# Optimization experiments

Measured on AMD Instinct MI355X. Metric: run time of the kernel, lower is better.

## Reference

```python
import jax, jax.numpy as jnp
import numpy as np

B, S0 = 16, 511
D = 512    # encoder_output_dim
HG = 256   # graph_rnn_hidden_graph
HE = 256   # graph_rnn_hidden_edge (must equal HG: h_prev[0] = graph_state)
T = 128    # tag_representation_dim
M = 32     # graph_rnn_m
S = S0 + 1 # after head-sentinel prepend


def setup_inputs() -> dict:
    ks = iter(jax.random.split(jax.random.key(0), 40))
    def U(shape, fan):
        # torch RNN/Linear default init: U(-1/sqrt(fan), 1/sqrt(fan))
        return jax.random.uniform(next(ks), shape, jnp.float32, -1.0, 1.0) / np.sqrt(fan)
    return {
        'input': jax.random.normal(next(ks), (B, S0, D), jnp.float32),
        'sentinel': jax.random.normal(next(ks), (D,), jnp.float32),
        'g_Wih0': U((HG, D), HG), 'g_Whh0': U((HG, HG), HG), 'g_bih0': U((HG,), HG), 'g_bhh0': U((HG,), HG),
        'g_Wih1': U((HG, HG), HG), 'g_Whh1': U((HG, HG), HG), 'g_bih1': U((HG,), HG), 'g_bhh1': U((HG,), HG),
        'e_Wih0': U((HE, 1), HE), 'e_Whh0': U((HE, HE), HE), 'e_bih0': U((HE,), HE), 'e_bhh0': U((HE,), HE),
        'e_Wih1': U((HE, HE), HE), 'e_Whh1': U((HE, HE), HE), 'e_bih1': U((HE,), HE), 'e_bhh1': U((HE,), HE),
        'cls_W': U((1, HE), HE), 'cls_b': U((1,), HE),
        'head_W': U((T, HG), HG), 'head_b': U((T,), HG),
        'dep_W': U((T, HG), HG), 'dep_b': U((T,), HG),
        'mask': jnp.ones((B, S0), jnp.int32),
        'head_indices': jax.random.randint(next(ks), (B, S0), 0, S0, jnp.int32),
    }


def _rnn_layer(x, W_ih, W_hh, b_ih, b_hh):
    # Elman RNN layer (tanh), batch_first, h0 = 0. x: [B, S, Din] -> [B, S, H]
    xw = jnp.einsum('bsd,hd->bsh', x, W_ih) + b_ih + b_hh  # hoist input GEMM out of scan
    h0 = jnp.zeros((x.shape[0], W_hh.shape[0]), x.dtype)
    def step(h, xw_t):
        h = jnp.tanh(xw_t + h @ W_hh.T)
        return h, h
    _, ys = jax.lax.scan(step, h0, jnp.swapaxes(xw, 0, 1))
    return jnp.swapaxes(ys, 0, 1)


def _forward(input, sentinel, g_Wih0, g_Whh0, g_bih0, g_bhh0, g_Wih1, g_Whh1, g_bih1, g_bhh1,
             e_Wih0, e_Whh0, e_bih0, e_bhh0, e_Wih1, e_Whh1, e_bih1, e_bhh1,
             cls_W, cls_b, head_W, head_b, dep_W, dep_b, mask, head_indices):
    Bv = input.shape[0]
    # prepend head sentinel / prepend_ones
    x = jnp.concatenate([jnp.broadcast_to(sentinel, (Bv, 1, D)), input], axis=1)   # [B,S,D]
    mask_f = jnp.concatenate([jnp.ones((Bv, 1), mask.dtype), mask], axis=1)        # [B,S]
    # graph_pass: 2-layer tanh RNN; pad_packed_sequence zeroes padded timesteps
    h = _rnn_layer(x, g_Wih0, g_Whh0, g_bih0, g_bhh0)
    gs = _rnn_layer(h, g_Wih1, g_Whh1, g_bih1, g_bhh1)                             # [B,S,HG]
    gs = gs * mask_f[..., None].astype(gs.dtype)
    N = Bv * S
    gt = gs.reshape(N, HG)
    def estep(carry, _):
        xe, h0, h1 = carry
        h0 = jnp.tanh(xe @ e_Wih0.T + e_bih0 + e_bhh0 + h0 @ e_Whh0.T)
        h1 = jnp.tanh(h0 @ e_Wih1.T + e_bih1 + e_bhh1 + h1 @ e_Whh1.T)
        p = jax.nn.sigmoid(h1 @ cls_W.T + cls_b)   # [N,1]
        return (p, h0, h1), p[:, 0]
    init = (jnp.ones((N, 1), gs.dtype), gt, jnp.zeros((N, HE), gs.dtype))
    _, probs = jax.lax.scan(estep, init, None, length=M)                           # [M,N]
    A = jnp.concatenate([jnp.ones((1, N), gs.dtype), probs], axis=0).T.reshape(Bv, S, M + 1)
    # reshape_adj: scatter the M-band back into a [B,S,S] matrix, then transpose
    Ab = A[:, :, 1:]                                                               # [B,S,M]
    i = jnp.arange(S)[:, None]
    j = jnp.arange(S)[None, :]
    start = jnp.maximum(0, i - M)
    valid = (j >= start) & (j < i)
    midx = jnp.clip(j - start, 0, M - 1)                                           # [S,S]
    gathered = Ab[:, jnp.arange(S)[:, None], midx]                                 # [B,S,S]
    arc_logits = jnp.swapaxes(jnp.where(valid[None], gathered, jnp.zeros((), gs.dtype)), 1, 2)
    # tag heads (dropout = identity at inference)
    head_tag = jax.nn.elu(jnp.einsum('bsh,th->bst', gs, head_W) + head_b)
    dep_tag = jax.nn.elu(jnp.einsum('bsh,th->bst', gs, dep_W) + dep_b)
    return head_tag, dep_tag, arc_logits


def reference(input, sentinel, g_Wih0, g_Whh0, g_bih0, g_bhh0, g_Wih1, g_Whh1, g_bih1, g_bhh1,
              e_Wih0, e_Whh0, e_bih0, e_bhh0, e_Wih1, e_Whh1, e_bih1, e_bhh1,
              cls_W, cls_b, head_W, head_b, dep_W, dep_b, mask, head_indices):
    return _forward(input, sentinel, g_Wih0, g_Whh0, g_bih0, g_bhh0, g_Wih1, g_Whh1, g_bih1, g_bhh1,
                    e_Wih0, e_Whh0, e_bih0, e_bhh0, e_Wih1, e_Whh1, e_bih1, e_bhh1,
                    cls_W, cls_b, head_W, head_b, dep_W, dep_b, mask, head_indices)
```

## Files before the change

### kernel.cpp

```cpp
#include <hip/hip_runtime.h>

typedef unsigned short u16;
typedef short s8v __attribute__((ext_vector_type(8)));
typedef float f4v __attribute__((ext_vector_type(4)));

__device__ __forceinline__ float bf2f(u16 s) {
  unsigned u = ((unsigned)s) << 16;
  return __builtin_bit_cast(float, u);
}
__device__ __forceinline__ u16 f2bf(float f) {
  unsigned u = __builtin_bit_cast(unsigned, f);
  unsigned r = u + 0x7fffu + ((u >> 16) & 1u);
  return (u16)(r >> 16);
}
__device__ __forceinline__ s8v load8bf(const u16* p) {
  return __builtin_bit_cast(s8v, *(const uint4*)p);
}
__device__ __forceinline__ f4v mfma16(s8v a, s8v b, f4v c) {
  return __builtin_amdgcn_mfma_f32_16x16x32_bf16(a, b, c, 0, 0, 0);
}
__device__ __forceinline__ s8v pin8(s8v x) {
  union { s8v v; unsigned u[4]; } t;
  t.v = x;
  asm volatile("" : "+v"(t.u[0]), "+v"(t.u[1]), "+v"(t.u[2]), "+v"(t.u[3]));
  return t.v;
}
__device__ __forceinline__ void barrier_lds() {
  asm volatile("s_waitcnt lgkmcnt(0)\n\ts_barrier" ::: "memory");
}
__device__ __forceinline__ void cvt8(const float* p, s8v& hi, s8v& lo) {
  float4 x0 = ((const float4*)p)[0];
  float4 x1 = ((const float4*)p)[1];
  float v[8] = {x0.x, x0.y, x0.z, x0.w, x1.x, x1.y, x1.z, x1.w};
  union { s8v v; u16 a[8]; } H, L;
#pragma unroll
  for (int i = 0; i < 8; ++i) {
    u16 h = f2bf(v[i]);
    H.a[i] = h;
    L.a[i] = f2bf(v[i] - bf2f(h));
  }
  hi = H.v;
  lo = L.v;
}
__device__ __forceinline__ float fast_tanh(float x) {
  float t = __builtin_amdgcn_exp2f(x * 2.885390081777927f);
  return 1.f - 2.f * __builtin_amdgcn_rcpf(t + 1.f);
}
__device__ __forceinline__ float fast_sigmoid(float x) {
  float t = __builtin_amdgcn_exp2f(x * -1.4426950408889634f);
  return __builtin_amdgcn_rcpf(1.f + t);
}

__global__ void k_prep(const float* __restrict__ W0, const float* __restrict__ W1,
                       u16* __restrict__ whh0b, u16* __restrict__ whh1b,
                       const float* __restrict__ E0, const float* __restrict__ E1,
                       const float* __restrict__ E2, u16* __restrict__ B0,
                       u16* __restrict__ B1, u16* __restrict__ B2,
                       const float* __restrict__ gW0, u16* __restrict__ gw0hi,
                       u16* __restrict__ gw0lo, const float* __restrict__ gW1,
                       u16* __restrict__ gw1hi, u16* __restrict__ gw1lo,
                       const float* __restrict__ hW, u16* __restrict__ hWhi,
                       u16* __restrict__ hWlo, const float* __restrict__ dW,
                       u16* __restrict__ dWhi, u16* __restrict__ dWlo,
                       const int* __restrict__ mask, float* __restrict__ maskfb) {
  int t = blockIdx.x * 256 + threadIdx.x;
  if (t < 131072) {
    int layer = t >> 16;
    int idx = t & 65535;
    const float* W = layer ? W1 : W0;
    u16* dst = layer ? whh1b : whh0b;
    dst[idx] = f2bf(W[idx]);
  } else if (t < 327680) {
    int c = t - 131072;
    int which = c >> 16;
    int idx = c & 65535;
    const float* src = which == 0 ? E0 : (which == 1 ? E1 : E2);
    u16* dst = which == 0 ? B0 : (which == 1 ? B1 : B2);
    dst[idx] = f2bf(src[idx]);
  } else if (t < 589824) {
    const float* src;
    u16 *dhi, *dlo;
    int idx;
    if (t < 458752) { idx = t - 327680; src = gW0; dhi = gw0hi; dlo = gw0lo; }
    else if (t < 524288) { idx = t - 458752; src = gW1; dhi = gw1hi; dlo = gw1lo; }
    else if (t < 557056) { idx = t - 524288; src = hW; dhi = hWhi; dlo = hWlo; }
    else { idx = t - 557056; src = dW; dhi = dWhi; dlo = dWlo; }
    float v = src[idx];
    u16 h = f2bf(v);
    dhi[idx] = h;
    dlo[idx] = f2bf(v - bf2f(h));
  } else if (t < 598016) {
    int c = t - 589824;
    int s = c >> 4, b = c & 15;
    maskfb[c] = (s == 0) ? 1.f : (float)mask[b * 511 + s - 1];
  }
}

__launch_bounds__(256)
__global__ void k_xw0(const float* __restrict__ input, const float* __restrict__ sentinel,
                      const u16* __restrict__ Whi, const u16* __restrict__ Wlo,
                      const float* __restrict__ b1, const float* __restrict__ b2,
                      float* __restrict__ outxw) {
  const int l = threadIdx.x & 63;
  const int wv = threadIdx.x >> 6;
  const int l15 = l & 15, q = l >> 4;
  const int row0 = blockIdx.x * 64 + wv * 16;
  const int col0 = blockIdx.y * 64;
  int row = row0 + l15;
  int s = row & 511, b = row >> 9;
  const float* aptr = (s == 0) ? sentinel : input + (((size_t)(b * 511 + s - 1)) << 9);
  f4v acc[4];
#pragma unroll
  for (int i = 0; i < 4; ++i) acc[i] = (f4v){0.f, 0.f, 0.f, 0.f};
#pragma unroll
  for (int kt = 0; kt < 16; ++kt) {
    int k0 = kt * 32 + q * 8;
    s8v ah, al;
    cvt8(aptr + k0, ah, al);
#pragma unroll
    for (int nt = 0; nt < 4; ++nt) {
      int j = col0 + nt * 16 + l15;
      s8v wh = load8bf(Whi + ((size_t)j << 9) + k0);
      s8v wl = load8bf(Wlo + ((size_t)j << 9) + k0);
      acc[nt] = mfma16(ah, wh, acc[nt]);
      acc[nt] = mfma16(al, wh, acc[nt]);
      acc[nt] = mfma16(ah, wl, acc[nt]);
    }
  }
#pragma unroll
  for (int nt = 0; nt < 4; ++nt) {
    int col = col0 + nt * 16 + l15;
    float bias = b1[col] + b2[col];
#pragma unroll
    for (int r = 0; r < 4; ++r) {
      int rr = row0 + q * 4 + r;
      outxw[((size_t)rr << 8) + col] = acc[nt][r] + bias;
    }
  }
}

__launch_bounds__(256)
__global__ void k_gemm(const float* __restrict__ A, const u16* __restrict__ Whi,
                       const u16* __restrict__ Wlo, const float* __restrict__ b1,
                       const float* __restrict__ b2, float* __restrict__ outf,
                       int K, int J, int act) {
  const int l = threadIdx.x & 63;
  const int wv = threadIdx.x >> 6;
  const int l15 = l & 15, q = l >> 4;
  const int row0 = blockIdx.x * 64 + wv * 16;
  const int col0 = blockIdx.y * 64;
  const float* aptr = A + (size_t)(row0 + l15) * K;
  f4v acc[4];
#pragma unroll
  for (int i = 0; i < 4; ++i) acc[i] = (f4v){0.f, 0.f, 0.f, 0.f};
  const int nkt = K >> 5;
  for (int kt = 0; kt < nkt; ++kt) {
    int k0 = kt * 32 + q * 8;
    s8v ah, al;
    cvt8(aptr + k0, ah, al);
#pragma unroll
    for (int nt = 0; nt < 4; ++nt) {
      int j = col0 + nt * 16 + l15;
      s8v wh = load8bf(Whi + (size_t)j * K + k0);
      s8v wl = load8bf(Wlo + (size_t)j * K + k0);
      acc[nt] = mfma16(ah, wh, acc[nt]);
      acc[nt] = mfma16(al, wh, acc[nt]);
      acc[nt] = mfma16(ah, wl, acc[nt]);
    }
  }
#pragma unroll
  for (int nt = 0; nt < 4; ++nt) {
    int col = col0 + nt * 16 + l15;
    float bias = b1[col] + (b2 ? b2[col] : 0.f);
#pragma unroll
    for (int r = 0; r < 4; ++r) {
      int rr = row0 + q * 4 + r;
      float v = acc[nt][r] + bias;
      if (act) v = v > 0.f ? v : (__builtin_amdgcn_exp2f(v * 1.4426950408889634f) - 1.f);
      outf[(size_t)rr * J + col] = v;
    }
  }
}

__launch_bounds__(256, 1)
__global__ void k_scan_m(const float* __restrict__ xw, const u16* __restrict__ Wb,
                         float* __restrict__ outf, const float* __restrict__ maskf) {
  __shared__ u16 H[2][272];
  __shared__ float mtab[512];
  const int tid = threadIdx.x;
  const int l = tid & 63, wv = tid >> 6;
  const int l15 = l & 15, q = l >> 4;
  const int b = blockIdx.x;

  s8v w[4][8];
#pragma unroll
  for (int nt = 0; nt < 4; ++nt) {
    int j = wv * 64 + nt * 16 + l15;
#pragma unroll
    for (int kt = 0; kt < 8; ++kt)
      w[nt][kt] = pin8(load8bf(Wb + (j << 8) + kt * 32 + q * 8));
  }
  if (tid < 256) H[0][tid] = 0;
  for (int c = tid; c < 512; c += 256)
    mtab[c] = maskf ? maskf[c * 16 + b] : 1.f;
  __syncthreads();

  const size_t nbase = (size_t)b << 9;
  const float* xrow = xw + (nbase << 8);
  const int j0 = wv * 64 + l15;
  const int q0 = (q == 0);

  float xA[4], xB[4];
#pragma unroll
  for (int nt = 0; nt < 4; ++nt) {
    xA[nt] = xrow[j0 + nt * 16];
    xB[nt] = xrow[256 + j0 + nt * 16];
  }

  auto STEP = [&](int s, int par, float* xc) {
    const u16* Hr = &H[par][0];
    f4v acc[4];
#pragma unroll
    for (int nt = 0; nt < 4; ++nt) acc[nt] = (f4v){xc[nt], 0.f, 0.f, 0.f};
#pragma unroll
    for (int kt = 0; kt < 8; ++kt) {
      s8v ha = load8bf(Hr + kt * 32 + q * 8);
#pragma unroll
      for (int nt = 0; nt < 4; ++nt) acc[nt] = mfma16(ha, w[nt][kt], acc[nt]);
    }
    float mf = mtab[s];
    u16* Hw = &H[1 - par][0];
    float* orow = outf + ((nbase + s) << 8);
#pragma unroll
    for (int nt = 0; nt < 4; ++nt) {
      float h = fast_tanh(acc[nt][0]);
      if (q0) {
        Hw[j0 + nt * 16] = f2bf(h);
        orow[j0 + nt * 16] = h * mf;
      }
    }
  };

  for (int s = 0; s < 512; s += 2) {
    STEP(s, 0, xA);
    int sp = s + 2; if (sp > 511) sp = 511;
#pragma unroll
    for (int nt = 0; nt < 4; ++nt) xA[nt] = xrow[(sp << 8) + j0 + nt * 16];
    barrier_lds();
    STEP(s + 1, 1, xB);
    int sq = s + 3; if (sq > 511) sq = 511;
#pragma unroll
    for (int nt = 0; nt < 4; ++nt) xB[nt] = xrow[(sq << 8) + j0 + nt * 16];
    barrier_lds();
  }
}

__launch_bounds__(512, 2)
__global__ void k_enc(const float* __restrict__ gs,
                      const u16* __restrict__ W0b, const u16* __restrict__ W1b,
                      const u16* __restrict__ W2b, const float* __restrict__ wih0,
                      const float* __restrict__ bih0, const float* __restrict__ bhh0,
                      const float* __restrict__ bih1, const float* __restrict__ bhh1,
                      const float* __restrict__ clsW, const float* __restrict__ clsb,
                      float* __restrict__ Ab) {
  __shared__ __align__(16) u16 hA0[32 * 264];
  __shared__ __align__(16) u16 hA1[32 * 264];
  __shared__ float xe[32];
  __shared__ float b0v[256], w0v[256], b1v[256], clsv[256];
  __shared__ float clsbs;
  const int tid = threadIdx.x;
  const int n0 = blockIdx.x * 32;

  for (int c = tid; c < 8192; c += 512) {
    int row = c >> 8, col = c & 255;
    hA0[row * 264 + col] = f2bf(gs[(((size_t)(n0 + row)) << 8) + col]);
    hA1[row * 264 + col] = 0;
  }
  if (tid < 256) {
    b0v[tid] = bih0[tid] + bhh0[tid];
    w0v[tid] = wih0[tid];
    b1v[tid] = bih1[tid] + bhh1[tid];
    clsv[tid] = clsW[tid];
  }
  if (tid < 32) xe[tid] = 1.0f;
  if (tid == 0) clsbs = clsb[0];

  const int l = tid & 63, wv = tid >> 6;
  const int l15 = l & 15, q = l >> 4;
  const int colbase = wv * 32;

  s8v w0[2][8], w1[2][8], w2[2][8];
#pragma unroll
  for (int nt = 0; nt < 2; ++nt) {
    int jj = colbase + nt * 16 + l15;
#pragma unroll
    for (int kt = 0; kt < 8; ++kt) {
      int off = (jj << 8) + kt * 32 + q * 8;
      w0[nt][kt] = load8bf(W0b + off);
      w1[nt][kt] = load8bf(W1b + off);
      w2[nt][kt] = load8bf(W2b + off);
    }
  }
  __syncthreads();

  for (int m = 0; m < 32; ++m) {
    f4v acc[2][2];
#pragma unroll
    for (int mt = 0; mt < 2; ++mt)
#pragma unroll
      for (int nt = 0; nt < 2; ++nt) acc[mt][nt] = (f4v){0.f, 0.f, 0.f, 0.f};
#pragma unroll
    for (int kt = 0; kt < 8; ++kt) {
#pragma unroll
      for (int mt = 0; mt < 2; ++mt) {
        s8v a = __builtin_bit_cast(s8v, *(const uint4*)&hA0[(mt * 16 + l15) * 264 + kt * 32 + q * 8]);
        acc[mt][0] = mfma16(a, w0[0][kt], acc[mt][0]);
        acc[mt][1] = mfma16(a, w0[1][kt], acc[mt][1]);
      }
    }
    __syncthreads();
#pragma unroll
    for (int nt = 0; nt < 2; ++nt) {
      int col = colbase + nt * 16 + l15;
      float wc = w0v[col], bc = b0v[col];
#pragma unroll
      for (int mt = 0; mt < 2; ++mt)
#pragma unroll
        for (int r = 0; r < 4; ++r) {
          int row = mt * 16 + q * 4 + r;
          float v = acc[mt][nt][r] + xe[row] * wc + bc;
          hA0[row * 264 + col] = f2bf(fast_tanh(v));
        }
    }
    __syncthreads();
#pragma unroll
    for (int mt = 0; mt < 2; ++mt)
#pragma unroll
      for (int nt = 0; nt < 2; ++nt) acc[mt][nt] = (f4v){0.f, 0.f, 0.f, 0.f};
#pragma unroll
    for (int kt = 0; kt < 8; ++kt) {
#pragma unroll
      for (int mt = 0; mt < 2; ++mt) {
        s8v a0 = __builtin_bit_cast(s8v, *(const uint4*)&hA0[(mt * 16 + l15) * 264 + kt * 32 + q * 8]);
        s8v a1 = __builtin_bit_cast(s8v, *(const uint4*)&hA1[(mt * 16 + l15) * 264 + kt * 32 + q * 8]);
        acc[mt][0] = mfma16(a0, w1[0][kt], acc[mt][0]);
        acc[mt][1] = mfma16(a0, w1[1][kt], acc[mt][1]);
        acc[mt][0] = mfma16(a1, w2[0][kt], acc[mt][0]);
        acc[mt][1] = mfma16(a1, w2[1][kt], acc[mt][1]);
      }
    }
    __syncthreads();
#pragma unroll
    for (int nt = 0; nt < 2; ++nt) {
      int col = colbase + nt * 16 + l15;
      float bc = b1v[col];
#pragma unroll
      for (int mt = 0; mt < 2; ++mt)
#pragma unroll
        for (int r = 0; r < 4; ++r) {
          int row = mt * 16 + q * 4 + r;
          float v = acc[mt][nt][r] + bc;
          hA1[row * 264 + col] = f2bf(fast_tanh(v));
        }
    }
    __syncthreads();
    if (tid < 256) {
      int row = tid >> 3, seg = tid & 7;
      float sum = 0.f;
#pragma unroll
      for (int u = 0; u < 4; ++u) {
        int col = seg * 32 + u * 8;
#pragma unroll
        for (int e = 0; e < 8; ++e) sum += bf2f(hA1[row * 264 + col + e]) * clsv[col + e];
      }
      sum += __shfl_down(sum, 4, 8);
      sum += __shfl_down(sum, 2, 8);
      sum += __shfl_down(sum, 1, 8);
      if (seg == 0) {
        float pp = fast_sigmoid(sum + clsbs);
        xe[row] = pp;
        Ab[(((size_t)(n0 + row)) << 5) + m] = pp;
      }
    }
    __syncthreads();
  }
}

__global__ void k_arc(const float* __restrict__ Ab, float* __restrict__ out2) {
  int t = blockIdx.x * 256 + threadIdx.x;
  int b = t >> 18;
  int rem = t & 262143;
  int j = rem >> 9, i = rem & 511;
  int start = i - 32;
  if (start < 0) start = 0;
  float v = 0.f;
  if (j >= start && j < i) v = Ab[((((size_t)b << 9) + i) << 5) + (j - start)];
  out2[t] = v;
}

extern "C" void kernel_launch(void* const* d_in, const int* in_sizes, int n_in,
                              void* d_out, int out_size, void* d_ws, size_t ws_size,
                              hipStream_t stream) {
  const float* input    = (const float*)d_in[0];
  const float* sentinel = (const float*)d_in[1];
  const float* g_Wih0   = (const float*)d_in[2];
  const float* g_Whh0   = (const float*)d_in[3];
  const float* g_bih0   = (const float*)d_in[4];
  const float* g_bhh0   = (const float*)d_in[5];
  const float* g_Wih1   = (const float*)d_in[6];
  const float* g_Whh1   = (const float*)d_in[7];
  const float* g_bih1   = (const float*)d_in[8];
  const float* g_bhh1   = (const float*)d_in[9];
  const float* e_Wih0   = (const float*)d_in[10];
  const float* e_Whh0   = (const float*)d_in[11];
  const float* e_bih0   = (const float*)d_in[12];
  const float* e_bhh0   = (const float*)d_in[13];
  const float* e_Wih1   = (const float*)d_in[14];
  const float* e_Whh1   = (const float*)d_in[15];
  const float* e_bih1   = (const float*)d_in[16];
  const float* e_bhh1   = (const float*)d_in[17];
  const float* cls_W    = (const float*)d_in[18];
  const float* cls_b    = (const float*)d_in[19];
  const float* head_W   = (const float*)d_in[20];
  const float* head_b   = (const float*)d_in[21];
  const float* dep_W    = (const float*)d_in[22];
  const float* dep_b    = (const float*)d_in[23];
  const int* mask       = (const int*)d_in[24];

  float* out = (float*)d_out;
  char* ws = (char*)d_ws;
  float* xw_buf = (float*)ws;
  float* hseq   = (float*)(ws + (8u << 20));
  float* gsb    = (float*)(ws + (16u << 20));
  float* Ab     = (float*)(ws + (24u << 20));
  size_t o = (25u << 20);
  u16* whh0b   = (u16*)(ws + o); o += 128u << 10;
  u16* whh1b   = (u16*)(ws + o); o += 128u << 10;
  float* maskfb= (float*)(ws + o); o += 32u << 10;
  u16* eb0     = (u16*)(ws + o); o += 128u << 10;
  u16* eb1     = (u16*)(ws + o); o += 128u << 10;
  u16* eb2     = (u16*)(ws + o); o += 128u << 10;
  u16* gw0hi   = (u16*)(ws + o); o += 256u << 10;
  u16* gw0lo   = (u16*)(ws + o); o += 256u << 10;
  u16* gw1hi   = (u16*)(ws + o); o += 128u << 10;
  u16* gw1lo   = (u16*)(ws + o); o += 128u << 10;
  u16* hWhi    = (u16*)(ws + o); o += 64u << 10;
  u16* hWlo    = (u16*)(ws + o); o += 64u << 10;
  u16* dWhi    = (u16*)(ws + o); o += 64u << 10;
  u16* dWlo    = (u16*)(ws + o); o += 64u << 10;

  k_prep<<<2336, 256, 0, stream>>>(g_Whh0, g_Whh1, whh0b, whh1b, e_Whh0, e_Wih1, e_Whh1,
                                   eb0, eb1, eb2, g_Wih0, gw0hi, gw0lo, g_Wih1, gw1hi,
                                   gw1lo, head_W, hWhi, hWlo, dep_W, dWhi, dWlo,
                                   mask, maskfb);
  k_xw0<<<dim3(128, 4), 256, 0, stream>>>(input, sentinel, gw0hi, gw0lo, g_bih0, g_bhh0,
                                          xw_buf);
  k_scan_m<<<16, 256, 0, stream>>>(xw_buf, whh0b, hseq, nullptr);
  k_gemm<<<dim3(128, 4), 256, 0, stream>>>(hseq, gw1hi, gw1lo, g_bih1, g_bhh1, xw_buf,
                                           256, 256, 0);
  k_scan_m<<<16, 256, 0, stream>>>(xw_buf, whh1b, gsb, maskfb);
  k_gemm<<<dim3(128, 2), 256, 0, stream>>>(gsb, hWhi, hWlo, head_b, nullptr, out,
                                           256, 128, 1);
  k_gemm<<<dim3(128, 2), 256, 0, stream>>>(gsb, dWhi, dWlo, dep_b, nullptr, out + 1048576,
                                           256, 128, 1);
  k_enc<<<256, 512, 0, stream>>>(gsb, eb0, eb1, eb2, e_Wih0, e_bih0, e_bhh0,
                                 e_bih1, e_bhh1, cls_W, cls_b, Ab);
  k_arc<<<16384, 256, 0, stream>>>(Ab, out + 2097152);
}
```

Measured before the change: 961.8 us.

## Fuse both graph RNN layers into one wavefront-pipelined scan kernel

Replaces the two sequential layer scans and the intermediate input-projection GEMM with a single kernel that runs layer 0 and layer 1 in a skewed pipeline. Each step computes layer-0's recurrence, layer-1's input projection from the fresh layer-0 state, and layer-1's recurrence for an earlier timestep, passing values through LDS. This removes one serial 512-step scan and the GEMM plus its global round trip, at the cost of three times the MFMA work per step and triple the register-resident weights, which may raise register pressure. The layer-1 input projection now uses only the high bf16 part of the weights instead of the hi/lo split, lowering precision.

```diff
diff --git a/kernel.cpp b/kernel.cpp
--- a/kernel.cpp
+++ b/kernel.cpp
@@ -183,31 +183,46 @@
 }
 
 __launch_bounds__(256, 1)
-__global__ void k_scan_m(const float* __restrict__ xw, const u16* __restrict__ Wb,
+__global__ void k_scan_f(const float* __restrict__ xw, const u16* __restrict__ W0b,
+                         const u16* __restrict__ Wxb, const u16* __restrict__ W1b,
+                         const float* __restrict__ bih1, const float* __restrict__ bhh1,
                          float* __restrict__ outf, const float* __restrict__ maskf) {
-  __shared__ u16 H[2][272];
+  __shared__ u16 H1[2][272];
+  __shared__ u16 H2[2][272];
+  __shared__ float XW2[2][272];
   __shared__ float mtab[512];
   const int tid = threadIdx.x;
   const int l = tid & 63, wv = tid >> 6;
   const int l15 = l & 15, q = l >> 4;
   const int b = blockIdx.x;
 
-  s8v w[4][8];
+  s8v w0[4][8], wx[4][8], w1[4][8];
 #pragma unroll
   for (int nt = 0; nt < 4; ++nt) {
     int j = wv * 64 + nt * 16 + l15;
 #pragma unroll
-    for (int kt = 0; kt < 8; ++kt)
-      w[nt][kt] = pin8(load8bf(Wb + (j << 8) + kt * 32 + q * 8));
-  }
-  if (tid < 256) H[0][tid] = 0;
-  for (int c = tid; c < 512; c += 256)
-    mtab[c] = maskf ? maskf[c * 16 + b] : 1.f;
+    for (int kt = 0; kt < 8; ++kt) {
+      int off = (j << 8) + kt * 32 + q * 8;
+      w0[nt][kt] = pin8(load8bf(W0b + off));
+      wx[nt][kt] = pin8(load8bf(Wxb + off));
+      w1[nt][kt] = pin8(load8bf(W1b + off));
+    }
+  }
+  if (tid < 256) {
+    H1[0][tid] = 0; H1[1][tid] = 0;
+    H2[0][tid] = 0; H2[1][tid] = 0;
+    XW2[0][tid] = 0.f; XW2[1][tid] = 0.f;
+  }
+  for (int c = tid; c < 512; c += 256) mtab[c] = maskf[c * 16 + b];
+
+  const int j0 = wv * 64 + l15;
+  float b2v[4];
+#pragma unroll
+  for (int nt = 0; nt < 4; ++nt) b2v[nt] = bih1[j0 + nt * 16] + bhh1[j0 + nt * 16];
   __syncthreads();
 
   const size_t nbase = (size_t)b << 9;
   const float* xrow = xw + (nbase << 8);
-  const int j0 = wv * 64 + l15;
   const int q0 = (q == 0);
 
   float xA[4], xB[4];
@@ -217,38 +232,69 @@
     xB[nt] = xrow[256 + j0 + nt * 16];
   }
 
-  auto STEP = [&](int s, int par, float* xc) {
-    const u16* Hr = &H[par][0];
-    f4v acc[4];
-#pragma unroll
-    for (int nt = 0; nt < 4; ++nt) acc[nt] = (f4v){xc[nt], 0.f, 0.f, 0.f};
+  auto STEP = [&](int g, int par, float* xc) {
+    const u16* H1r = &H1[par][0];
+    const u16* H2r = &H2[par][0];
+    f4v a1[4], ax[4], a2[4];
+#pragma unroll
+    for (int nt = 0; nt < 4; ++nt) {
+      a1[nt] = (f4v){xc[nt], 0.f, 0.f, 0.f};
+      ax[nt] = (f4v){b2v[nt], 0.f, 0.f, 0.f};
+      a2[nt] = (f4v){XW2[par][j0 + nt * 16], 0.f, 0.f, 0.f};
+    }
 #pragma unroll
     for (int kt = 0; kt < 8; ++kt) {
-      s8v ha = load8bf(Hr + kt * 32 + q * 8);
-#pragma unroll
-      for (int nt = 0; nt < 4; ++nt) acc[nt] = mfma16(ha, w[nt][kt], acc[nt]);
-    }
-    float mf = mtab[s];
-    u16* Hw = &H[1 - par][0];
-    float* orow = outf + ((nbase + s) << 8);
-#pragma unroll
-    for (int nt = 0; nt < 4; ++nt) {
-      float h = fast_tanh(acc[nt][0]);
-      if (q0) {
-        Hw[j0 + nt * 16] = f2bf(h);
-        orow[j0 + nt * 16] = h * mf;
+      s8v h1b = load8bf(H1r + kt * 32 + q * 8);
+#pragma unroll
+      for (int nt = 0; nt < 4; ++nt) {
+        a1[nt] = mfma16(h1b, w0[nt][kt], a1[nt]);
+        ax[nt] = mfma16(h1b, wx[nt][kt], ax[nt]);
+      }
+    }
+#pragma unroll
+    for (int kt = 0; kt < 8; ++kt) {
+      s8v h2b = load8bf(H2r + kt * 32 + q * 8);
+#pragma unroll
+      for (int nt = 0; nt < 4; ++nt) a2[nt] = mfma16(h2b, w1[nt][kt], a2[nt]);
+    }
+    if (g < 512) {
+      u16* Hw = &H1[1 - par][0];
+#pragma unroll
+      for (int nt = 0; nt < 4; ++nt) {
+        float h = fast_tanh(a1[nt][0]);
+        if (q0) Hw[j0 + nt * 16] = f2bf(h);
+      }
+    }
+    if (g >= 1 && g < 513) {
+      float* Xw = &XW2[1 - par][0];
+#pragma unroll
+      for (int nt = 0; nt < 4; ++nt)
+        if (q0) Xw[j0 + nt * 16] = ax[nt][0];
+    }
+    if (g >= 2) {
+      int t = g - 2;
+      float mf = mtab[t];
+      u16* Hw = &H2[1 - par][0];
+      float* orow = outf + ((nbase + t) << 8);
+#pragma unroll
+      for (int nt = 0; nt < 4; ++nt) {
+        float h = fast_tanh(a2[nt][0]);
+        if (q0) {
+          Hw[j0 + nt * 16] = f2bf(h);
+          orow[j0 + nt * 16] = h * mf;
+        }
       }
     }
   };
 
-  for (int s = 0; s < 512; s += 2) {
-    STEP(s, 0, xA);
-    int sp = s + 2; if (sp > 511) sp = 511;
+  for (int g = 0; g < 514; g += 2) {
+    STEP(g, 0, xA);
+    int sp = g + 2; if (sp > 511) sp = 511;
 #pragma unroll
     for (int nt = 0; nt < 4; ++nt) xA[nt] = xrow[(sp << 8) + j0 + nt * 16];
     barrier_lds();
-    STEP(s + 1, 1, xB);
-    int sq = s + 3; if (sq > 511) sq = 511;
+    STEP(g + 1, 1, xB);
+    int sq = g + 3; if (sq > 511) sq = 511;
 #pragma unroll
     for (int nt = 0; nt < 4; ++nt) xB[nt] = xrow[(sq << 8) + j0 + nt * 16];
     barrier_lds();
@@ -430,7 +476,6 @@
   float* out = (float*)d_out;
   char* ws = (char*)d_ws;
   float* xw_buf = (float*)ws;
-  float* hseq   = (float*)(ws + (8u << 20));
   float* gsb    = (float*)(ws + (16u << 20));
   float* Ab     = (float*)(ws + (24u << 20));
   size_t o = (25u << 20);
@@ -455,10 +500,8 @@
                                    mask, maskfb);
   k_xw0<<<dim3(128, 4), 256, 0, stream>>>(input, sentinel, gw0hi, gw0lo, g_bih0, g_bhh0,
                                           xw_buf);
-  k_scan_m<<<16, 256, 0, stream>>>(xw_buf, whh0b, hseq, nullptr);
-  k_gemm<<<dim3(128, 4), 256, 0, stream>>>(hseq, gw1hi, gw1lo, g_bih1, g_bhh1, xw_buf,
-                                           256, 256, 0);
-  k_scan_m<<<16, 256, 0, stream>>>(xw_buf, whh1b, gsb, maskfb);
+  k_scan_f<<<16, 256, 0, stream>>>(xw_buf, whh0b, gw1hi, whh1b, g_bih1, g_bhh1,
+                                   gsb, maskfb);
   k_gemm<<<dim3(128, 2), 256, 0, stream>>>(gsb, hWhi, hWlo, head_b, nullptr, out,
                                            256, 128, 1);
   k_gemm<<<dim3(128, 2), 256, 0, stream>>>(gsb, dWhi, dWlo, dep_b, nullptr, out + 1048576,
```

New measurement: 1.176 ms. 22.3% more time.
